# Performance work log

Hardware: AMD Instinct MI355X
Metric: run time of the kernel (lower is better)

Reference implementation:

```python
import jax, jax.numpy as jnp
import numpy as np

N_NODES = 100000
N_EDGES = 3200000


def setup_inputs() -> dict:
    key = jax.random.key(0)
    ks = jax.random.split(key, 12)
    x = jax.random.normal(ks[0], (N_NODES, 5), dtype=jnp.float32)
    edges = jax.random.randint(ks[1], (2, N_EDGES), 0, N_NODES)
    edge_attr = jax.random.normal(ks[2], (N_EDGES, 2), dtype=jnp.float32)
    detector_labels = jax.random.bernoulli(ks[3], 0.7, (N_NODES,))

    def init(k, shape, fan_in):
        return (jax.random.normal(k, shape, dtype=jnp.float32) / np.sqrt(fan_in)).astype(jnp.float32)

    W_gat = init(ks[4], (5, 16), 5)        # GATConv lin (shared src/dst)
    att_src = init(ks[5], (16,), 16)
    att_dst = init(ks[6], (16,), 16)
    W_edge = init(ks[7], (2, 16), 2)       # GATConv lin_edge
    att_edge = init(ks[8], (16,), 16)
    b_gat = jnp.zeros((16,), jnp.float32)
    W1 = init(ks[9], (34, 64), 34)
    b1 = jnp.zeros((64,), jnp.float32)
    W2 = init(ks[10], (64, 2), 64)
    b2 = jnp.zeros((2,), jnp.float32)
    return dict(x=x, edges=edges, edge_attr=edge_attr, detector_labels=detector_labels,
                W_gat=W_gat, att_src=att_src, att_dst=att_dst, W_edge=W_edge,
                att_edge=att_edge, b_gat=b_gat, W1=W1, b1=b1, W2=W2, b2=b2)


def reference(x, edges, edge_attr, detector_labels, W_gat, att_src, att_dst,
              W_edge, att_edge, b_gat, W1, b1, W2, b2):
    n_nodes = x.shape[0]
    src, dst = edges[0], edges[1]

    # --- GATConv(5 -> 16, heads=1, concat=False, edge_dim=2, no self loops) ---
    h = x @ W_gat                                        # [N, 16]
    a_src = h @ att_src                                  # [N]
    a_dst = h @ att_dst                                  # [N]
    a_edge = (edge_attr @ W_edge) @ att_edge             # [E]
    alpha = jax.nn.leaky_relu(a_src[src] + a_dst[dst] + a_edge, 0.2)
    # segmented softmax over incoming edges of each dst node
    seg_max = jax.ops.segment_max(alpha, dst, num_segments=n_nodes)
    ex = jnp.exp(alpha - seg_max[dst])
    denom = jax.ops.segment_sum(ex, dst, num_segments=n_nodes)
    a = ex / (denom[dst] + 1e-16)                        # [E]
    out = jax.ops.segment_sum(h[src] * a[:, None], dst, num_segments=n_nodes) + b_gat
    xh = jax.nn.relu(out)                                # [N, 16]

    # --- edge update: gather-concat-MLP ---
    feat = jnp.concatenate([xh[src], edge_attr, xh[dst]], axis=-1)   # [E, 34]
    ef = jax.nn.relu(feat @ W1 + b1) @ W2 + b2                       # [E, 2]

    # --- SplitSyndromes: keep edges whose both endpoints are detectors ---
    valid = detector_labels[src] & detector_labels[dst]
    idx = jnp.nonzero(valid)[0]        # eager (data-dependent size, not jitted)
    return edges[:, idx], jax.nn.sigmoid(ef[idx])
```

## Files before the change

### kernel.cpp

```cpp
#include <hip/hip_runtime.h>

#define NN 100000
#define NE 3200000
#define CH 8192
#define NCB ((NE + CH - 1) / CH)
#define ITER (CH / 256)
#define ITS (CH / 512)
#define NBK ((NN + 63) >> 6)
#define CAP 2560
#define NWG (NE / 64)

typedef __attribute__((ext_vector_type(8))) __bf16 bf16x8;
typedef __attribute__((ext_vector_type(4))) float f32x4;

union BF8 { unsigned short u[8]; bf16x8 v; };

__global__ void kdetect(const unsigned char* __restrict__ lab8, int* __restrict__ flags) {
  __shared__ int tmp[256];
  int t = threadIdx.x;
  int s = 0;
  for (int i = t; i < 25000; i += 256) s += lab8[4 * i + 1];
  tmp[t] = s;
  __syncthreads();
  for (int d = 128; d > 0; d >>= 1) { if (t < d) tmp[t] += tmp[t + d]; __syncthreads(); }
  if (t == 0) flags[0] = (tmp[0] != 0) ? 1 : 0;
}

__global__ void klab(const void* __restrict__ lab, const int* __restrict__ flags,
                     int* __restrict__ labN) {
  int n = blockIdx.x * 256 + threadIdx.x;
  if (n >= NN) return;
  int v;
  if (flags[0]) v = ((const unsigned char*)lab)[n];
  else          v = ((const int*)lab)[n];
  labN[n] = (v != 0) ? 1 : 0;
}

__global__ void kc01(const float* __restrict__ We, const float* __restrict__ ae,
                     float* __restrict__ c01) {
  if (threadIdx.x == 0) {
    float c0 = 0.f, c1 = 0.f;
    for (int k = 0; k < 16; k++) { c0 += We[k] * ae[k]; c1 += We[16 + k] * ae[k]; }
    c01[0] = c0; c01[1] = c1;
  }
}

__global__ void knodeA(const float* __restrict__ x, const float* __restrict__ Wg,
                       const float* __restrict__ atts, const float* __restrict__ attd,
                       float* __restrict__ a_src, float* __restrict__ a_dst) {
  int n = blockIdx.x * 256 + threadIdx.x;
  if (n >= NN) return;
  float xi[5];
#pragma unroll
  for (int i = 0; i < 5; i++) xi[i] = x[n * 5 + i];
  float asum = 0.f, dsum = 0.f;
#pragma unroll
  for (int k = 0; k < 16; k++) {
    float acc = 0.f;
#pragma unroll
    for (int i = 0; i < 5; i++) acc += xi[i] * Wg[i * 16 + k];
    asum += acc * atts[k];
    dsum += acc * attd[k];
  }
  a_src[n] = asum; a_dst[n] = dsum;
}

__global__ __launch_bounds__(256) void khist(const int* __restrict__ src,
                                             const int* __restrict__ dst,
                                             const int* __restrict__ labN,
                                             int* __restrict__ blkcnt,
                                             int* __restrict__ cntw,
                                             int* __restrict__ cntc) {
  __shared__ int hist[NBK];
  __shared__ int vsum;
  int tid = threadIdx.x, b = blockIdx.x;
  for (int i = tid; i < NBK; i += 256) hist[i] = 0;
  if (tid == 0) vsum = 0;
  __syncthreads();
  int lane = tid & 63, wid = tid >> 6;
  int wsum = 0;
  for (int it = 0; it < ITER; ++it) {
    int e = b * CH + it * 256 + tid;
    int v = 0;
    if (e < NE) {
      int s = src[e], d = dst[e];
      atomicAdd(&hist[d >> 6], 1);
      v = labN[s] & labN[d];
    }
    unsigned long long m = __ballot(v != 0);
    int c = __popcll(m);
    if (lane == 0) {
      int wg = b * 128 + it * 4 + wid;
      if (wg < NWG) cntw[wg] = c;
      wsum += c;
    }
  }
  if (lane == 0) atomicAdd(&vsum, wsum);
  __syncthreads();
  for (int i = tid; i < NBK; i += 256) blkcnt[i * NCB + b] = hist[i];
  if (tid == 0) cntc[b] = vsum;
}

__global__ __launch_bounds__(256) void kscanb(int* __restrict__ blkcnt,
                                              int* __restrict__ total) {
  __shared__ int a[512];
  int row = blockIdx.x, t = threadIdx.x;
  int* p = blkcnt + row * NCB;
  int o0 = (t < NCB) ? p[t] : 0;
  int o1 = (t + 256 < NCB) ? p[t + 256] : 0;
  a[t] = o0; a[t + 256] = o1;
  __syncthreads();
  for (int d = 1; d < 512; d <<= 1) {
    int x0 = (t >= d) ? a[t - d] : 0;
    int x1 = (t + 256 >= d) ? a[t + 256 - d] : 0;
    __syncthreads();
    a[t] += x0; a[t + 256] += x1;
    __syncthreads();
  }
  if (t < NCB) p[t] = a[t] - o0;
  if (t + 256 < NCB) p[t + 256] = a[t + 256] - o1;
  if (t == 0) total[row] = a[NCB - 1];
}

__global__ void kscan(const int* __restrict__ cnt, int* __restrict__ off, int nb) {
  __shared__ int tmp[256];
  __shared__ int carry;
  int t = threadIdx.x;
  if (t == 0) carry = 0;
  __syncthreads();
  for (int base = 0; base < nb; base += 256) {
    int i = base + t;
    int v = (i < nb) ? cnt[i] : 0;
    tmp[t] = v;
    __syncthreads();
    for (int d = 1; d < 256; d <<= 1) {
      int add = (t >= d) ? tmp[t - d] : 0;
      __syncthreads();
      tmp[t] += add;
      __syncthreads();
    }
    if (i < nb) off[i] = carry + tmp[t] - v;
    __syncthreads();
    if (t == 0) carry += tmp[255];
    __syncthreads();
  }
  if (t == 0) off[nb] = carry;
}

__global__ __launch_bounds__(128) void kscanw(const int* __restrict__ cntw,
                                              const int* __restrict__ offc,
                                              int* __restrict__ offw) {
  int b = blockIdx.x, t = threadIdx.x;
  __shared__ int a[128];
  int wg = b * 128 + t;
  int val = (wg < NWG) ? cntw[wg] : 0;
  a[t] = val;
  __syncthreads();
  for (int d = 1; d < 128; d <<= 1) {
    int x = (t >= d) ? a[t - d] : 0;
    __syncthreads();
    a[t] += x;
    __syncthreads();
  }
  if (wg < NWG) offw[wg] = offc[b] + a[t] - val;
}

__global__ __launch_bounds__(512) void kscat(
    const int* __restrict__ src, const int* __restrict__ dst,
    const float* __restrict__ eattr, const int* __restrict__ labN,
    const float* __restrict__ a_src, const float* __restrict__ a_dst,
    const float* __restrict__ c01, const int* __restrict__ bucket_base,
    const int* __restrict__ blkcnt, const int* __restrict__ offw,
    uint2* __restrict__ bins, float* __restrict__ out,
    float2* __restrict__ eat2, int NV) {
  __shared__ int cur[NBK];
  int b = blockIdx.x, tid = threadIdx.x;
  for (int i = tid; i < NBK; i += 512) cur[i] = bucket_base[i] + blkcnt[i * NCB + b];
  float c0 = c01[0], c1 = c01[1];
  __syncthreads();
  int lane = tid & 63, wid = tid >> 6;
  for (int it = 0; it < ITS; ++it) {
    int e = b * CH + it * 512 + tid;
    if (e >= NE) break;
    int s = src[e], d = dst[e];
    float2 ea = ((const float2*)eattr)[e];
    float al = a_src[s] + a_dst[d] + ea.x * c0 + ea.y * c1;
    al = (al > 0.f) ? al : 0.2f * al;
    float exv = __expf(al);
    int pos = atomicAdd(&cur[d >> 6], 1);
    uint2 pl;
    pl.x = ((unsigned)s << 6) | (unsigned)(d & 63);
    pl.y = __float_as_uint(exv);
    bins[pos] = pl;
    int v = labN[s] & labN[d];
    unsigned long long m = __ballot(v != 0);
    if (v) {
      int wg = b * 128 + it * 8 + wid;
      int p = offw[wg] + __popcll(m & ((1ull << lane) - 1ull));
      if (p < NV) {
        out[p] = (float)s;
        out[NV + p] = (float)d;
        eat2[p] = ea;
      }
    }
  }
}

__global__ __launch_bounds__(512) void kagg(
    const uint2* __restrict__ bins, const int* __restrict__ bucket_base,
    const float* __restrict__ x, const float* __restrict__ Wg,
    const float* __restrict__ bg, float* __restrict__ xh) {
  __shared__ uint2 pay[CAP];
  __shared__ int cnt[64], inc[64], cur[64];
  __shared__ float sWg[80], sbg[16];
  int k = blockIdx.x, tid = threadIdx.x;
  if (tid < 80) sWg[tid] = Wg[tid];
  else if (tid < 96) sbg[tid - 80] = bg[tid - 80];
  int start = bucket_base[k], end = bucket_base[k + 1];
  int node0 = k << 6;
  int c = tid & 15, g = tid >> 4;
  __syncthreads();
  float w0 = sWg[c], w1 = sWg[16 + c], w2 = sWg[32 + c], w3 = sWg[48 + c], w4 = sWg[64 + c];
  float acc[2] = {0.f, 0.f}, den[2] = {0.f, 0.f};
  for (int cb = start; cb < end; cb += CAP) {
    int n = min(end - cb, CAP);
    if (tid < 64) cnt[tid] = 0;
    __syncthreads();
    uint2 st0, st1, st2, st3, st4;
    {
      int i;
      i = tid;          if (i < n) { st0 = bins[cb + i]; atomicAdd(&cnt[st0.x & 63], 1); }
      i = tid + 512;    if (i < n) { st1 = bins[cb + i]; atomicAdd(&cnt[st1.x & 63], 1); }
      i = tid + 1024;   if (i < n) { st2 = bins[cb + i]; atomicAdd(&cnt[st2.x & 63], 1); }
      i = tid + 1536;   if (i < n) { st3 = bins[cb + i]; atomicAdd(&cnt[st3.x & 63], 1); }
      i = tid + 2048;   if (i < n) { st4 = bins[cb + i]; atomicAdd(&cnt[st4.x & 63], 1); }
    }
    __syncthreads();
    if (tid < 64) inc[tid] = cnt[tid];
    __syncthreads();
    for (int d = 1; d < 64; d <<= 1) {
      int v = 0;
      if (tid >= d && tid < 64) v = inc[tid - d];
      __syncthreads();
      if (tid < 64) inc[tid] += v;
      __syncthreads();
    }
    if (tid < 64) cur[tid] = inc[tid] - cnt[tid];
    __syncthreads();
    {
      int i;
      i = tid;          if (i < n) pay[atomicAdd(&cur[st0.x & 63], 1)] = st0;
      i = tid + 512;    if (i < n) pay[atomicAdd(&cur[st1.x & 63], 1)] = st1;
      i = tid + 1024;   if (i < n) pay[atomicAdd(&cur[st2.x & 63], 1)] = st2;
      i = tid + 1536;   if (i < n) pay[atomicAdd(&cur[st3.x & 63], 1)] = st3;
      i = tid + 2048;   if (i < n) pay[atomicAdd(&cur[st4.x & 63], 1)] = st4;
    }
    __syncthreads();
#pragma unroll
    for (int p = 0; p < 2; ++p) {
      int nd = p * 32 + g;
      int re = inc[nd], rs = re - cnt[nd];
      float a = 0.f, ds = 0.f;
      for (int idx = rs; idx < re; ++idx) {
        uint2 pl = pay[idx];
        int s = (int)(pl.x >> 6);
        float exv = __uint_as_float(pl.y);
        const float* xp = x + s * 5;
        float h = xp[0] * w0 + xp[1] * w1 + xp[2] * w2 + xp[3] * w3 + xp[4] * w4;
        a += h * exv;
        ds += exv;
      }
      acc[p] += a; den[p] += ds;
    }
    __syncthreads();
  }
#pragma unroll
  for (int p = 0; p < 2; ++p) {
    int node = node0 + p * 32 + g;
    if (node < NN) {
      float dn = fmaxf(den[p], 1e-30f);
      float v = acc[p] / dn + sbg[c];
      xh[node * 16 + c] = (v > 0.f) ? v : 0.f;
    }
  }
}

__global__ __launch_bounds__(256) void kmlp(
    const float2* __restrict__ eat2, const float* __restrict__ xh,
    const float* __restrict__ W1, const float* __restrict__ b1,
    const float* __restrict__ W2, const float* __restrict__ b2,
    float* __restrict__ out, int NV) {
  int tid = threadIdx.x;
  int lane = tid & 63, wid = tid >> 6;
  int lo4 = lane & 15, q = lane >> 4;

  BF8 bh[4], bl[4];
#pragma unroll
  for (int ct = 0; ct < 4; ct++) {
    int col = ct * 16 + lo4;
#pragma unroll
    for (int i = 0; i < 8; i++) {
      int k = q * 8 + i;
      int r = (k < 16) ? k : (k + 2);
      float w = W1[r * 64 + col];
      unsigned u = __float_as_uint(w);
      float rem = w - __uint_as_float(u & 0xffff0000u);
      bh[ct].u[i] = (unsigned short)(u >> 16);
      bl[ct].u[i] = (unsigned short)(__float_as_uint(rem) >> 16);
    }
  }
  float b1v[4], w16v[4], w17v[4], w2a[4], w2b[4];
#pragma unroll
  for (int ct = 0; ct < 4; ct++) {
    int j = ct * 16 + lo4;
    b1v[ct] = b1[j];
    w16v[ct] = W1[16 * 64 + j];
    w17v[ct] = W1[17 * 64 + j];
    w2a[ct] = W2[j * 2 + 0];
    w2b[ct] = W2[j * 2 + 1];
  }
  float bias20 = b2[0], bias21 = b2[1];

  int nwaves = gridDim.x * 4;
  int ntiles = (NV + 15) >> 4;
  for (int tb = blockIdx.x * 4 + wid; tb < ntiles; tb += nwaves) {
    int base = tb * 16;
    BF8 ah, al;
    {
      int p = base + lo4;
      float vals[8] = {0.f, 0.f, 0.f, 0.f, 0.f, 0.f, 0.f, 0.f};
      if (p < NV) {
        int node = (int)out[((q < 2) ? 0 : NV) + p];
        const float4* xp = (const float4*)(xh + node * 16 + (q & 1) * 8);
        float4 f0 = xp[0], f1 = xp[1];
        vals[0] = f0.x; vals[1] = f0.y; vals[2] = f0.z; vals[3] = f0.w;
        vals[4] = f1.x; vals[5] = f1.y; vals[6] = f1.z; vals[7] = f1.w;
      }
#pragma unroll
      for (int i = 0; i < 8; i++) {
        unsigned u = __float_as_uint(vals[i]);
        float rem = vals[i] - __uint_as_float(u & 0xffff0000u);
        ah.u[i] = (unsigned short)(u >> 16);
        al.u[i] = (unsigned short)(__float_as_uint(rem) >> 16);
      }
    }
    f32x4 acc[4];
#pragma unroll
    for (int ct = 0; ct < 4; ct++) {
      f32x4 z = {0.f, 0.f, 0.f, 0.f};
      z = __builtin_amdgcn_mfma_f32_16x16x32_bf16(ah.v, bh[ct].v, z, 0, 0, 0);
      z = __builtin_amdgcn_mfma_f32_16x16x32_bf16(ah.v, bl[ct].v, z, 0, 0, 0);
      z = __builtin_amdgcn_mfma_f32_16x16x32_bf16(al.v, bh[ct].v, z, 0, 0, 0);
      acc[ct] = z;
    }
    float o0[4], o1[4];
#pragma unroll
    for (int reg = 0; reg < 4; reg++) {
      int pr = base + q * 4 + reg;
      float2 ea = make_float2(0.f, 0.f);
      if (pr < NV) ea = eat2[pr];
      float s0 = 0.f, s1 = 0.f;
#pragma unroll
      for (int ct = 0; ct < 4; ct++) {
        float h = acc[ct][reg] + b1v[ct] + ea.x * w16v[ct] + ea.y * w17v[ct];
        h = fmaxf(h, 0.f);
        s0 += h * w2a[ct];
        s1 += h * w2b[ct];
      }
      o0[reg] = s0; o1[reg] = s1;
    }
#pragma unroll
    for (int m = 1; m < 16; m <<= 1) {
#pragma unroll
      for (int reg = 0; reg < 4; reg++) {
        o0[reg] += __shfl_xor(o0[reg], m, 64);
        o1[reg] += __shfl_xor(o1[reg], m, 64);
      }
    }
    if (lo4 == 0) {
#pragma unroll
      for (int reg = 0; reg < 4; reg++) {
        int pr = base + q * 4 + reg;
        if (pr < NV) {
          float v0 = bias20 + o0[reg], v1 = bias21 + o1[reg];
          ((float2*)(out + 2 * (size_t)NV))[pr] = make_float2(
              1.f / (1.f + __expf(-v0)), 1.f / (1.f + __expf(-v1)));
        }
      }
    }
  }
}

static inline size_t al64(size_t v) { return (v + 63) & ~(size_t)63; }

extern "C" void kernel_launch(void* const* d_in, const int* in_sizes, int n_in,
                              void* d_out, int out_size, void* d_ws, size_t ws_size,
                              hipStream_t stream) {
  const float* x     = (const float*)d_in[0];
  const int*   edges = (const int*)d_in[1];
  const float* eattr = (const float*)d_in[2];
  const void*  labels= d_in[3];
  const float* Wg    = (const float*)d_in[4];
  const float* atts  = (const float*)d_in[5];
  const float* attd  = (const float*)d_in[6];
  const float* We    = (const float*)d_in[7];
  const float* atte  = (const float*)d_in[8];
  const float* bg    = (const float*)d_in[9];
  const float* W1    = (const float*)d_in[10];
  const float* b1    = (const float*)d_in[11];
  const float* W2    = (const float*)d_in[12];
  const float* b2    = (const float*)d_in[13];
  float* out = (float*)d_out;
  const int NV = out_size / 4;
  const int* src = edges;
  const int* dst = edges + NE;

  char* w = (char*)d_ws;
  float* xh    = (float*)w;   w += al64((size_t)NN * 64);
  uint2* bins  = (uint2*)w;   w += al64((size_t)NE * 8);
  float2* eat2 = (float2*)w;  w += al64((size_t)NV * 8);
  float* a_src = (float*)w;   w += al64((size_t)NN * 4);
  float* a_dst = (float*)w;   w += al64((size_t)NN * 4);
  int* labN    = (int*)w;     w += al64((size_t)NN * 4);
  int* blkcnt  = (int*)w;     w += al64((size_t)NBK * NCB * 4);
  int* total   = (int*)w;     w += al64((size_t)NBK * 4);
  int* bb      = (int*)w;     w += al64((size_t)(NBK + 1) * 4);
  int* cntc    = (int*)w;     w += al64((size_t)NCB * 4);
  int* offc    = (int*)w;     w += al64((size_t)(NCB + 1) * 4);
  int* cntw    = (int*)w;     w += al64((size_t)NWG * 4);
  int* offw    = (int*)w;     w += al64((size_t)NWG * 4);
  float* c01   = (float*)w;   w += 64;
  int* flags   = (int*)w;     w += 64;

  kdetect<<<1, 256, 0, stream>>>((const unsigned char*)labels, flags);
  klab<<<(NN + 255) / 256, 256, 0, stream>>>(labels, flags, labN);
  kc01<<<1, 64, 0, stream>>>(We, atte, c01);
  knodeA<<<(NN + 255) / 256, 256, 0, stream>>>(x, Wg, atts, attd, a_src, a_dst);
  khist<<<NCB, 256, 0, stream>>>(src, dst, labN, blkcnt, cntw, cntc);
  kscanb<<<NBK, 256, 0, stream>>>(blkcnt, total);
  kscan<<<1, 256, 0, stream>>>(total, bb, NBK);
  kscan<<<1, 256, 0, stream>>>(cntc, offc, NCB);
  kscanw<<<NCB, 128, 0, stream>>>(cntw, offc, offw);
  kscat<<<NCB, 512, 0, stream>>>(src, dst, eattr, labN, a_src, a_dst, c01, bb,
                                 blkcnt, offw, bins, out, eat2, NV);
  kagg<<<NBK, 512, 0, stream>>>(bins, bb, x, Wg, bg, xh);
  if (NV > 0)
    kmlp<<<2048, 256, 0, stream>>>(eat2, xh, W1, b1, W2, b2, out, NV);
}
```

Baseline: 297.9 us.

## Shrink edge chunks, transpose bucket counts, strip-scan columns, pack node attention with labels

Cuts the edge chunk size from 8192 to 2048, giving four times as many histogram/scatter blocks. The per-chunk bucket counts are stored chunk-major and scanned with a two-level strip scan in place of a per-bucket shared-memory scan. Node attention scalars are packed with the detector label into float2 so the scatter kernel does one gather per endpoint instead of two. Scatter blocks are remapped so consecutive chunks land on the same XCD. The finer chunks raise parallelism and cut per-block shared-atomic contention, at the cost of a larger count matrix and more blocks each initialising the 1563-entry cursor array.

```diff
diff --git a/kernel.cpp b/kernel.cpp
--- a/kernel.cpp
+++ b/kernel.cpp
@@ -2,13 +2,14 @@
 
 #define NN 100000
 #define NE 3200000
-#define CH 8192
+#define CH 2048
 #define NCB ((NE + CH - 1) / CH)
 #define ITER (CH / 256)
-#define ITS (CH / 512)
 #define NBK ((NN + 63) >> 6)
 #define CAP 2560
 #define NWG (NE / 64)
+#define NSTRIP 8
+#define SLEN ((NCB + NSTRIP - 1) / NSTRIP)
 
 typedef __attribute__((ext_vector_type(8))) __bf16 bf16x8;
 typedef __attribute__((ext_vector_type(4))) float f32x4;
@@ -47,7 +48,8 @@
 
 __global__ void knodeA(const float* __restrict__ x, const float* __restrict__ Wg,
                        const float* __restrict__ atts, const float* __restrict__ attd,
-                       float* __restrict__ a_src, float* __restrict__ a_dst) {
+                       const int* __restrict__ labN,
+                       float2* __restrict__ pka, float2* __restrict__ pkd) {
   int n = blockIdx.x * 256 + threadIdx.x;
   if (n >= NN) return;
   float xi[5];
@@ -62,7 +64,9 @@
     asum += acc * atts[k];
     dsum += acc * attd[k];
   }
-  a_src[n] = asum; a_dst[n] = dsum;
+  float lab = labN[n] ? 1.f : 0.f;
+  pka[n] = make_float2(asum, lab);
+  pkd[n] = make_float2(dsum, lab);
 }
 
 __global__ __launch_bounds__(256) void khist(const int* __restrict__ src,
@@ -90,36 +94,47 @@
     unsigned long long m = __ballot(v != 0);
     int c = __popcll(m);
     if (lane == 0) {
-      int wg = b * 128 + it * 4 + wid;
+      int wg = b * (CH / 64) + it * 4 + wid;
       if (wg < NWG) cntw[wg] = c;
       wsum += c;
     }
   }
   if (lane == 0) atomicAdd(&vsum, wsum);
   __syncthreads();
-  for (int i = tid; i < NBK; i += 256) blkcnt[i * NCB + b] = hist[i];
+  int* row = blkcnt + (size_t)b * NBK;
+  for (int i = tid; i < NBK; i += 256) row[i] = hist[i];
   if (tid == 0) cntc[b] = vsum;
 }
 
-__global__ __launch_bounds__(256) void kscanb(int* __restrict__ blkcnt,
-                                              int* __restrict__ total) {
-  __shared__ int a[512];
-  int row = blockIdx.x, t = threadIdx.x;
-  int* p = blkcnt + row * NCB;
-  int o0 = (t < NCB) ? p[t] : 0;
-  int o1 = (t + 256 < NCB) ? p[t + 256] : 0;
-  a[t] = o0; a[t + 256] = o1;
-  __syncthreads();
-  for (int d = 1; d < 512; d <<= 1) {
-    int x0 = (t >= d) ? a[t - d] : 0;
-    int x1 = (t + 256 >= d) ? a[t + 256 - d] : 0;
-    __syncthreads();
-    a[t] += x0; a[t + 256] += x1;
-    __syncthreads();
-  }
-  if (t < NCB) p[t] = a[t] - o0;
-  if (t + 256 < NCB) p[t + 256] = a[t + 256] - o1;
-  if (t == 0) total[row] = a[NCB - 1];
+__global__ __launch_bounds__(256) void kscanc1(int* __restrict__ blkcnt,
+                                               int* __restrict__ ssum) {
+  int i = blockIdx.x * 256 + threadIdx.x;
+  int st = blockIdx.y;
+  if (i >= NBK) return;
+  int c0 = st * SLEN, c1 = min(c0 + SLEN, NCB);
+  int run = 0;
+#pragma unroll 4
+  for (int c = c0; c < c1; c++) {
+    int* p = blkcnt + (size_t)c * NBK + i;
+    int v = *p;
+    *p = run;
+    run += v;
+  }
+  ssum[st * NBK + i] = run;
+}
+
+__global__ __launch_bounds__(256) void kscanc2(int* __restrict__ ssum,
+                                               int* __restrict__ total) {
+  int i = blockIdx.x * 256 + threadIdx.x;
+  if (i >= NBK) return;
+  int run = 0;
+#pragma unroll
+  for (int st = 0; st < NSTRIP; st++) {
+    int v = ssum[st * NBK + i];
+    ssum[st * NBK + i] = run;
+    run += v;
+  }
+  total[i] = run;
 }
 
 __global__ void kscan(const int* __restrict__ cnt, int* __restrict__ off, int nb) {
@@ -150,41 +165,49 @@
 __global__ __launch_bounds__(128) void kscanw(const int* __restrict__ cntw,
                                               const int* __restrict__ offc,
                                               int* __restrict__ offw) {
-  int b = blockIdx.x, t = threadIdx.x;
   __shared__ int a[128];
-  int wg = b * 128 + t;
+  int t = threadIdx.x;
+  int wg = blockIdx.x * 128 + t;
+  int l = t & 31;
   int val = (wg < NWG) ? cntw[wg] : 0;
   a[t] = val;
   __syncthreads();
-  for (int d = 1; d < 128; d <<= 1) {
-    int x = (t >= d) ? a[t - d] : 0;
+  for (int d = 1; d < 32; d <<= 1) {
+    int x = (l >= d) ? a[t - d] : 0;
     __syncthreads();
     a[t] += x;
     __syncthreads();
   }
-  if (wg < NWG) offw[wg] = offc[b] + a[t] - val;
-}
-
-__global__ __launch_bounds__(512) void kscat(
+  if (wg < NWG) offw[wg] = offc[wg >> 5] + a[t] - val;
+}
+
+__global__ __launch_bounds__(256) void kscat(
     const int* __restrict__ src, const int* __restrict__ dst,
-    const float* __restrict__ eattr, const int* __restrict__ labN,
-    const float* __restrict__ a_src, const float* __restrict__ a_dst,
+    const float* __restrict__ eattr,
+    const float2* __restrict__ pka, const float2* __restrict__ pkd,
     const float* __restrict__ c01, const int* __restrict__ bucket_base,
-    const int* __restrict__ blkcnt, const int* __restrict__ offw,
+    const int* __restrict__ blkcnt, const int* __restrict__ ssum,
+    const int* __restrict__ offw,
     uint2* __restrict__ bins, float* __restrict__ out,
     float2* __restrict__ eat2, int NV) {
   __shared__ int cur[NBK];
-  int b = blockIdx.x, tid = threadIdx.x;
-  for (int i = tid; i < NBK; i += 512) cur[i] = bucket_base[i] + blkcnt[i * NCB + b];
+  int ob = blockIdx.x, tid = threadIdx.x;
+  int xcd = ob & 7, loc = ob >> 3;
+  const int q = NCB >> 3, r = NCB & 7;
+  int b = ((xcd < r) ? xcd * (q + 1) : r * (q + 1) + (xcd - r) * q) + loc;
+  const int* bc = blkcnt + (size_t)b * NBK;
+  const int* ss = ssum + (size_t)(b / SLEN) * NBK;
+  for (int i = tid; i < NBK; i += 256) cur[i] = bucket_base[i] + ss[i] + bc[i];
   float c0 = c01[0], c1 = c01[1];
   __syncthreads();
   int lane = tid & 63, wid = tid >> 6;
-  for (int it = 0; it < ITS; ++it) {
-    int e = b * CH + it * 512 + tid;
+  for (int it = 0; it < ITER; ++it) {
+    int e = b * CH + it * 256 + tid;
     if (e >= NE) break;
     int s = src[e], d = dst[e];
     float2 ea = ((const float2*)eattr)[e];
-    float al = a_src[s] + a_dst[d] + ea.x * c0 + ea.y * c1;
+    float2 ga = pka[s], gd = pkd[d];
+    float al = ga.x + gd.x + ea.x * c0 + ea.y * c1;
     al = (al > 0.f) ? al : 0.2f * al;
     float exv = __expf(al);
     int pos = atomicAdd(&cur[d >> 6], 1);
@@ -192,10 +215,10 @@
     pl.x = ((unsigned)s << 6) | (unsigned)(d & 63);
     pl.y = __float_as_uint(exv);
     bins[pos] = pl;
-    int v = labN[s] & labN[d];
-    unsigned long long m = __ballot(v != 0);
+    int v = (ga.y != 0.f) && (gd.y != 0.f);
+    unsigned long long m = __ballot(v);
     if (v) {
-      int wg = b * 128 + it * 8 + wid;
+      int wg = b * (CH / 64) + it * 4 + wid;
       int p = offw[wg] + __popcll(m & ((1ull << lane) - 1ull));
       if (p < NV) {
         out[p] = (float)s;
@@ -419,10 +442,11 @@
   float* xh    = (float*)w;   w += al64((size_t)NN * 64);
   uint2* bins  = (uint2*)w;   w += al64((size_t)NE * 8);
   float2* eat2 = (float2*)w;  w += al64((size_t)NV * 8);
-  float* a_src = (float*)w;   w += al64((size_t)NN * 4);
-  float* a_dst = (float*)w;   w += al64((size_t)NN * 4);
+  float2* pka  = (float2*)w;  w += al64((size_t)NN * 8);
+  float2* pkd  = (float2*)w;  w += al64((size_t)NN * 8);
   int* labN    = (int*)w;     w += al64((size_t)NN * 4);
-  int* blkcnt  = (int*)w;     w += al64((size_t)NBK * NCB * 4);
+  int* blkcnt  = (int*)w;     w += al64((size_t)NCB * NBK * 4);
+  int* ssum    = (int*)w;     w += al64((size_t)NSTRIP * NBK * 4);
   int* total   = (int*)w;     w += al64((size_t)NBK * 4);
   int* bb      = (int*)w;     w += al64((size_t)(NBK + 1) * 4);
   int* cntc    = (int*)w;     w += al64((size_t)NCB * 4);
@@ -435,14 +459,15 @@
   kdetect<<<1, 256, 0, stream>>>((const unsigned char*)labels, flags);
   klab<<<(NN + 255) / 256, 256, 0, stream>>>(labels, flags, labN);
   kc01<<<1, 64, 0, stream>>>(We, atte, c01);
-  knodeA<<<(NN + 255) / 256, 256, 0, stream>>>(x, Wg, atts, attd, a_src, a_dst);
+  knodeA<<<(NN + 255) / 256, 256, 0, stream>>>(x, Wg, atts, attd, labN, pka, pkd);
   khist<<<NCB, 256, 0, stream>>>(src, dst, labN, blkcnt, cntw, cntc);
-  kscanb<<<NBK, 256, 0, stream>>>(blkcnt, total);
+  kscanc1<<<dim3((NBK + 255) / 256, NSTRIP), 256, 0, stream>>>(blkcnt, ssum);
+  kscanc2<<<(NBK + 255) / 256, 256, 0, stream>>>(ssum, total);
   kscan<<<1, 256, 0, stream>>>(total, bb, NBK);
   kscan<<<1, 256, 0, stream>>>(cntc, offc, NCB);
-  kscanw<<<NCB, 128, 0, stream>>>(cntw, offc, offw);
-  kscat<<<NCB, 512, 0, stream>>>(src, dst, eattr, labN, a_src, a_dst, c01, bb,
-                                 blkcnt, offw, bins, out, eat2, NV);
+  kscanw<<<(NWG + 127) / 128, 128, 0, stream>>>(cntw, offc, offw);
+  kscat<<<NCB, 256, 0, stream>>>(src, dst, eattr, pka, pkd, c01, bb, blkcnt, ssum,
+                                 offw, bins, out, eat2, NV);
   kagg<<<NBK, 512, 0, stream>>>(bins, bb, x, Wg, bg, xh);
   if (NV > 0)
     kmlp<<<2048, 256, 0, stream>>>(eat2, xh, W1, b1, W2, b2, out, NV);
```

Result: no change. 294.2 us (-1.2%).
